# Kernel optimization log

Measured on AMD Instinct MI355X. Metric: run time of the kernel, lower is better.

The kernel has to match this reference:

```python
import jax, jax.numpy as jnp
import numpy as np

BATCH, SEQ, IN, HID, LAYERS = 128, 512, 512, 1024, 2


def setup_inputs() -> dict:
    key = jax.random.key(0)
    ks = jax.random.split(key, 8)
    s = 0.02
    # Gate weights concatenated in order [forget, input, output, cell]
    W0 = jax.random.normal(ks[0], (IN + HID, 4 * HID), dtype=jnp.float32) * s
    b0 = jax.random.normal(ks[1], (4 * HID,), dtype=jnp.float32) * s
    W1 = jax.random.normal(ks[2], (HID + HID, 4 * HID), dtype=jnp.float32) * s
    b1 = jax.random.normal(ks[3], (4 * HID,), dtype=jnp.float32) * s
    Wout = jax.random.normal(ks[4], (HID, 1), dtype=jnp.float32) * s
    bout = jax.random.normal(ks[5], (1,), dtype=jnp.float32) * s
    x = jax.random.normal(ks[6], (BATCH, SEQ, IN), dtype=jnp.float32)
    return {"x": x, "W0": W0, "b0": b0, "W1": W1, "b1": b1,
            "Wout": Wout, "bout": bout}


def _cell(x_in, h_prev, c_prev, W, b):
    z = jnp.concatenate([x_in, h_prev], axis=-1) @ W + b  # (B, 4H)
    f, i, o, g = jnp.split(z, 4, axis=-1)
    c_next = jax.nn.sigmoid(f) * c_prev + jax.nn.sigmoid(i) * jnp.tanh(g)
    h_next = jax.nn.sigmoid(o) * jnp.tanh(c_next)
    return h_next, c_next


def reference(x, W0, b0, W1, b1, Wout, bout):
    B = x.shape[0]
    H = W0.shape[1] // 4
    params = ((W0, b0), (W1, b1))

    h0 = tuple(jnp.zeros((B, H), x.dtype) for _ in range(LAYERS))
    c0 = tuple(jnp.zeros((B, H), x.dtype) for _ in range(LAYERS))

    def step(carry, x_t):
        h, c = carry
        inp = x_t
        new_h, new_c = [], []
        for l in range(LAYERS):
            W, b = params[l]
            h_n, c_n = _cell(inp, h[l], c[l], W, b)
            new_h.append(h_n)
            new_c.append(c_n)
            inp = h_n
        return (tuple(new_h), tuple(new_c)), None

    xs = jnp.swapaxes(x, 0, 1)  # (T, B, IN)
    (h_fin, _), _ = jax.lax.scan(step, (h0, c0), xs)
    last = h_fin[-1]  # output of top layer at last timestep
    logits = last @ Wout + bout  # (B, 1)
    return jax.nn.sigmoid(logits).squeeze(-1)  # (B,)
```

## Files before the change

### kernel.cpp

```cpp
#include <hip/hip_runtime.h>
#include <hip/hip_bf16.h>
#include <cstdint>
#include <cstddef>


#define BATCH 128
#define SEQ   512
#define INP   512
#define HID   1024
#define NCOL  4096
#define NB    256
#define KS0   48
#define KS1   64
#define HS_   (BATCH * HID)

typedef __bf16 bf16x8 __attribute__((ext_vector_type(8)));
typedef float  f32x4  __attribute__((ext_vector_type(4)));
typedef unsigned int u32x4 __attribute__((ext_vector_type(4)));
typedef unsigned long long u64;
typedef u64 u64x2 __attribute__((ext_vector_type(2)));

__device__ __forceinline__ bf16x8 load_bf16x8(const __hip_bfloat16* p) {
    u32x4 u = *reinterpret_cast<const u32x4*>(p);
    return __builtin_bit_cast(bf16x8, u);
}
__device__ __forceinline__ bf16x8 aload_bf16x8(const __hip_bfloat16* p) {
    u64x2 q;
    q[0] = __hip_atomic_load((const u64*)p,       __ATOMIC_RELAXED, __HIP_MEMORY_SCOPE_AGENT);
    q[1] = __hip_atomic_load((const u64*)(p + 4), __ATOMIC_RELAXED, __HIP_MEMORY_SCOPE_AGENT);
    return __builtin_bit_cast(bf16x8, q);
}
__device__ __forceinline__ f32x4 mfma16(bf16x8 a, bf16x8 b, f32x4 c) {
    return __builtin_amdgcn_mfma_f32_16x16x32_bf16(a, b, c, 0, 0, 0);
}
__device__ __forceinline__ float sigmoidf_(float x) {
    return 1.0f / (1.0f + __expf(-x));
}
__device__ __forceinline__ float tanhf_(float x) {
    return 1.0f - 2.0f / (__expf(2.0f * x) + 1.0f);
}
__device__ __forceinline__ void gload16(const void* g, void* l) {
    __builtin_amdgcn_global_load_lds(
        (const __attribute__((address_space(1))) uint32_t*)g,
        (__attribute__((address_space(3))) uint32_t*)l, 16, 0, 0);
}
#define VMWAIT asm volatile("s_waitcnt vmcnt(12)" ::: "memory")

template<int Ks>
__global__ __launch_bounds__(1024)
void pack_frag_kernel(const float* __restrict__ W, __hip_bfloat16* __restrict__ F)
{
    __shared__ float tile[32][33];
    const int k0 = blockIdx.x * 32;
    const int c0 = blockIdx.y * 32;
    const int tx = threadIdx.x & 31, ty = threadIdx.x >> 5;
    tile[ty][tx] = W[(size_t)(k0 + ty) * NCOL + (c0 + tx)];
    __syncthreads();
    const int cL  = threadIdx.x >> 5;
    const int kgw = (threadIdx.x >> 3) & 3;
    const int j   = threadIdx.x & 7;
    const int c   = c0 + cL;
    const int r   = (c & 1023) * 4 + (c >> 10);
    const int nb2 = r >> 4, cl = r & 15;
    const int ks  = k0 >> 5;
    const size_t chunk = ((size_t)(nb2 * Ks + ks) * 4 + kgw) * 16 + cl;
    F[chunk * 8 + j] = __float2bfloat16(tile[kgw * 8 + j][cL]);
}

__global__ void bias_reorder_kernel(const float* __restrict__ b0,
                                    const float* __restrict__ b1,
                                    float* __restrict__ b0r,
                                    float* __restrict__ b1r)
{
    int i = blockIdx.x * blockDim.x + threadIdx.x;
    if (i >= 2 * NCOL) return;
    const float* src = (i < NCOL) ? b0 : b1;
    float*       dst = (i < NCOL) ? b0r : b1r;
    int c = i & (NCOL - 1);
    dst[(c & 1023) * 4 + (c >> 10)] = src[c];
}

__global__ __launch_bounds__(256)
void xconv_kernel(const float* __restrict__ x, __hip_bfloat16* __restrict__ xb)
{
    const int idx = blockIdx.x * 256 + threadIdx.x;
    const int r   = idx & 63;
    const int kg  = (idx >> 6) & 3;
    const int mq  = (idx >> 8) & 1;
    const int ks  = (idx >> 9) & 15;
    const int t   = idx >> 13;
    const float* src = x + ((size_t)(mq * 64 + r) * SEQ + t) * INP + ks * 32 + kg * 8;
    bf16x8 v;
    #pragma unroll
    for (int j = 0; j < 8; ++j) v[j] = (__bf16)src[j];
    *reinterpret_cast<u32x4*>(xb + (size_t)idx * 8) = __builtin_bit_cast(u32x4, v);
}

__global__ __launch_bounds__(512, 2)
void lstm_persistent(const __hip_bfloat16* __restrict__ xb,
                     const __hip_bfloat16* __restrict__ F0,
                     const __hip_bfloat16* __restrict__ F1,
                     const float* __restrict__ b0r,
                     const float* __restrict__ b1r,
                     const float* __restrict__ Wout,
                     const float* __restrict__ bout,
                     __hip_bfloat16* __restrict__ h0r,
                     __hip_bfloat16* __restrict__ h1r,
                     float* __restrict__ out,
                     int* __restrict__ bar,
                     int rm, int fm)
{
    extern __shared__ char smem[];

    __shared__ float zacc[2][128][17];
    __shared__ float cS[2][512];
    __shared__ float biasS[2][16];
    __shared__ __hip_bfloat16 hstage[2][128][4];

    const int tid  = threadIdx.x;
    const int lane = tid & 63;
    const int wv   = tid >> 6;
    const int kq   = wv & 3;
    const int mq   = wv >> 2;
    const int lm   = lane & 15;
    const int kg   = lane >> 4;
    const int nb   = blockIdx.x;
    const uint32_t sbase = (uint32_t)wv * 16384;

    bf16x8 B0r_[12], B1r_[16];
    #pragma unroll
    for (int i = 0; i < 4; ++i)
        B0r_[i]     = load_bf16x8(F0 + ((((size_t)nb * KS0 + (4*kq + i)) * 4 + kg) * 16 + lm) * 8);
    #pragma unroll
    for (int i = 0; i < 8; ++i)
        B0r_[4 + i] = load_bf16x8(F0 + ((((size_t)nb * KS0 + (16 + 8*kq + i)) * 4 + kg) * 16 + lm) * 8);
    #pragma unroll
    for (int i = 0; i < 8; ++i)
        B1r_[i]     = load_bf16x8(F1 + ((((size_t)nb * KS1 + (8*kq + i)) * 4 + kg) * 16 + lm) * 8);
    #pragma unroll
    for (int i = 0; i < 8; ++i)
        B1r_[8 + i] = load_bf16x8(F1 + ((((size_t)nb * KS1 + (32 + 8*kq + i)) * 4 + kg) * 16 + lm) * 8);

    #pragma unroll
    for (int i = 0; i < 12; ++i) asm volatile("" : "+v"(B0r_[i]));
    #pragma unroll
    for (int i = 0; i < 16; ++i) asm volatile("" : "+v"(B1r_[i]));

    if (tid < 32) biasS[tid >> 4][tid & 15] = ((tid < 16) ? b0r : b1r)[nb * 16 + (tid & 15)];
    for (int i = tid; i < 1024; i += 512) cS[i >> 9][i & 511] = 0.f;
    for (int i = tid; i < 2 * 128 * 17; i += 512) ((float*)zacc)[i] = 0.f;
    __syncthreads();

    auto issueStep = [&](const __hip_bfloat16* src, int sl) {
        const char* g = (const char*)src + (size_t)lane * 16;
        char* l = smem + sbase + (uint32_t)sl * 4096;
        #pragma unroll
        for (int i2 = 0; i2 < 4; ++i2)
            gload16(g + i2 * 1024, l + i2 * 1024);
    };
    auto readA = [&](int sl, int f) -> bf16x8 {
        const char* lp = smem + sbase + (uint32_t)sl * 4096
                       + (uint32_t)kg * 1024 + (uint32_t)f * 256 + (uint32_t)lm * 16;
        u32x4 v = *(const u32x4*)lp;
        return __builtin_bit_cast(bf16x8, v);
    };

    #pragma unroll
    for (int s = 0; s < 4; ++s)
        issueStep(xb + ((size_t)((4*kq + s) * 2 + mq)) * 2048, s);

    for (int p = 0; p <= SEQ; ++p) {
        const __hip_bfloat16* h0p = h0r + (size_t)((p + rm)     & rm) * HS_;
        const __hip_bfloat16* h1p = h1r + (size_t)((p + rm - 1) & rm) * HS_;
        __hip_bfloat16*       h0w = h0r + (size_t)( p           & rm) * HS_;
        __hip_bfloat16*       h1w = h1r + (size_t)((p + rm)     & rm) * HS_;
        const int tn = (p + 1 < SEQ) ? (p + 1) : (SEQ - 1);

        f32x4 aL0[4], aL1[4];
        #pragma unroll
        for (int f = 0; f < 4; ++f) { aL0[f] = f32x4{0,0,0,0}; aL1[f] = f32x4{0,0,0,0}; }

        #pragma unroll
        for (int s = 0; s < 4; ++s) {
            VMWAIT;
            bf16x8 A[4];
            #pragma unroll
            for (int f = 0; f < 4; ++f) A[f] = readA(s, f);
            #pragma unroll
            for (int f = 0; f < 4; ++f) aL0[f] = mfma16(A[f], B0r_[s], aL0[f]);
            issueStep(h0p + ((size_t)((8*kq + s) * 2 + mq)) * 2048, s);
        }
        #pragma unroll
        for (int i = 0; i < 8; ++i) {
            VMWAIT;
            const int sl = (4 + i) & 3;
            bf16x8 A[4];
            #pragma unroll
            for (int f = 0; f < 4; ++f) A[f] = readA(sl, f);
            #pragma unroll
            for (int f = 0; f < 4; ++f) {
                aL0[f] = mfma16(A[f], B0r_[4 + i], aL0[f]);
                aL1[f] = mfma16(A[f], B1r_[i],     aL1[f]);
            }
            if (i < 4) issueStep(h0p + ((size_t)((8*kq + 4 + i)   * 2 + mq)) * 2048, (8 + i) & 3);
            else       issueStep(h1p + ((size_t)((8*kq + (i - 4)) * 2 + mq)) * 2048, (8 + i) & 3);
        }
        #pragma unroll
        for (int i = 0; i < 8; ++i) {
            VMWAIT;
            const int sl = (12 + i) & 3;
            bf16x8 A[4];
            #pragma unroll
            for (int f = 0; f < 4; ++f) A[f] = readA(sl, f);
            #pragma unroll
            for (int f = 0; f < 4; ++f) aL1[f] = mfma16(A[f], B1r_[8 + i], aL1[f]);
            if (i < 4)
                issueStep(h1p + ((size_t)((8*kq + 4 + i) * 2 + mq)) * 2048, (16 + i) & 3);
            else if (p < SEQ)
                issueStep(xb + (size_t)tn * 65536
                             + ((size_t)((4*kq + (i - 4)) * 2 + mq)) * 2048, (16 + i) & 3);
        }

        if (p < SEQ) {
            #pragma unroll
            for (int f = 0; f < 4; ++f)
                #pragma unroll
                for (int r = 0; r < 4; ++r)
                    atomicAdd(&zacc[0][mq*64 + f*16 + kg*4 + r][lm], aL0[f][r]);
        }
        if (p >= 1) {
            #pragma unroll
            for (int f = 0; f < 4; ++f)
                #pragma unroll
                for (int r = 0; r < 4; ++r)
                    atomicAdd(&zacc[1][mq*64 + f*16 + kg*4 + r][lm], aL1[f][r]);
        }
        __syncthreads();

        for (int it = tid; it < 1024; it += 512) {
            const int L   = it >> 9;
            const int idx = it & 511;
            const int bl  = idx >> 2;
            const int u   = idx & 3;
            const bool act = L ? (p >= 1) : (p < SEQ);
            if (act) {
                float* zb = &zacc[L][bl][4 * u];
                const float zf = zb[0] + biasS[L][4*u + 0];
                const float zi = zb[1] + biasS[L][4*u + 1];
                const float zo = zb[2] + biasS[L][4*u + 2];
                const float zg = zb[3] + biasS[L][4*u + 3];
                zb[0] = 0.f; zb[1] = 0.f; zb[2] = 0.f; zb[3] = 0.f;
                const float cold = cS[L][idx];
                const float cn = sigmoidf_(zf) * cold + sigmoidf_(zi) * tanhf_(zg);
                const float hn = sigmoidf_(zo) * tanhf_(cn);
                cS[L][idx] = cn;
                hstage[L][bl][u] = __float2bfloat16(hn);
            }
        }
        __syncthreads();

        if (tid < 256) {
            const int L  = tid >> 7;
            const int bl = tid & 127;
            const bool act = L ? (p >= 1) : (p < SEQ);
            if (act) {
                __hip_bfloat16* hw = L ? h1w : h0w;
                const int uks = nb >> 3, ukg = (nb >> 1) & 3, jb = (nb & 1) * 4;
                const int mqb = bl >> 6, rr = bl & 63;
                const size_t e = ((size_t)((uks*2 + mqb)*4 + ukg)*64 + rr)*8 + jb;
                const u64 v = *(const u64*)&hstage[L][bl][0];
                __hip_atomic_store((u64*)(hw + e), v,
                                   __ATOMIC_RELAXED, __HIP_MEMORY_SCOPE_AGENT);
            }
        }
        __syncthreads();

        if (tid == 0) {
            const int g = nb >> 5;
            int* arrv = bar + 32 * g;
            int* root = bar + 256;
            int* rel  = bar + 512 + 32 * g;
            const int e = p + 1;
            __hip_atomic_fetch_add(arrv, 1, __ATOMIC_RELAXED, __HIP_MEMORY_SCOPE_AGENT);
            if ((nb & 31) == 0) {
                while (__hip_atomic_load(arrv, __ATOMIC_RELAXED, __HIP_MEMORY_SCOPE_AGENT) < 32 * e)
                    __builtin_amdgcn_s_sleep(1);
                __hip_atomic_fetch_add(root, 1, __ATOMIC_RELAXED, __HIP_MEMORY_SCOPE_AGENT);
            }
            if (nb == 0) {
                while (__hip_atomic_load(root, __ATOMIC_RELAXED, __HIP_MEMORY_SCOPE_AGENT) < 8 * e)
                    __builtin_amdgcn_s_sleep(1);
                #pragma unroll
                for (int gg = 0; gg < 8; ++gg)
                    __hip_atomic_store(bar + 512 + 32 * gg, e,
                                       __ATOMIC_RELAXED, __HIP_MEMORY_SCOPE_AGENT);
            } else {
                while (__hip_atomic_load(rel, __ATOMIC_RELAXED, __HIP_MEMORY_SCOPE_AGENT) < e)
                    __builtin_amdgcn_s_sleep(2);
            }
            if ((p & fm) == fm)
                __builtin_amdgcn_fence(__ATOMIC_ACQUIRE, "agent");
            asm volatile("" ::: "memory");
        }
        __builtin_amdgcn_s_barrier();
    }

    if (nb == 0 && tid < BATCH) {
        const __hip_bfloat16* hb = h1r + (size_t)((SEQ - 1) & rm) * HS_;
        const int mqb = tid >> 6, rr = tid & 63;
        float acc = 0.f;
        for (int uu = 0; uu < HID; uu += 8) {
            const int uks = uu >> 5, ukg = (uu >> 3) & 3;
            const size_t e = ((size_t)((uks*2 + mqb)*4 + ukg)*64 + rr)*8;
            bf16x8 v = aload_bf16x8(hb + e);
            #pragma unroll
            for (int j = 0; j < 8; ++j) acc += (float)v[j] * Wout[uu + j];
        }
        out[tid] = 1.f / (1.f + __expf(-(acc + bout[0])));
    }
}

extern "C" void kernel_launch(void* const* d_in, const int* in_sizes, int n_in,
                              void* d_out, int out_size, void* d_ws, size_t ws_size,
                              hipStream_t stream)
{
    const float* x    = (const float*)d_in[0];
    const float* W0   = (const float*)d_in[1];
    const float* b0   = (const float*)d_in[2];
    const float* W1   = (const float*)d_in[3];
    const float* b1   = (const float*)d_in[4];
    const float* Wout = (const float*)d_in[5];
    const float* bout = (const float*)d_in[6];
    float* out = (float*)d_out;

    char* ws = (char*)d_ws;
    const size_t OFF_F0  = 0;
    const size_t OFF_F1  = 12582912;
    const size_t OFF_B0R = 29360128;
    const size_t OFF_B1R = 29376512;
    const size_t OFF_BAR = 29392896;
    const size_t OFF_R0  = 29396992;
    const size_t SLOT    = 262144;
    const size_t XBYTES  = (size_t)BATCH * SEQ * INP * 2;

    int rm, fm;
    if      (ws_size >= OFF_R0 + 128 * SLOT + XBYTES) { rm = 63; fm = 31; }
    else if (ws_size >= OFF_R0 +  32 * SLOT + XBYTES) { rm = 15; fm = 7;  }
    else                                              { rm = 1;  fm = 0;  }
    const size_t OFF_R1 = OFF_R0 + (size_t)(rm + 1) * SLOT;
    const size_t OFF_XB = OFF_R1 + (size_t)(rm + 1) * SLOT;

    __hip_bfloat16* F0  = (__hip_bfloat16*)(ws + OFF_F0);
    __hip_bfloat16* F1  = (__hip_bfloat16*)(ws + OFF_F1);
    float* b0r = (float*)(ws + OFF_B0R);
    float* b1r = (float*)(ws + OFF_B1R);
    __hip_bfloat16* h0r = (__hip_bfloat16*)(ws + OFF_R0);
    __hip_bfloat16* h1r = (__hip_bfloat16*)(ws + OFF_R1);
    int* bar = (int*)(ws + OFF_BAR);
    __hip_bfloat16* xbp = (__hip_bfloat16*)(ws + OFF_XB);

    hipMemsetAsync(ws + OFF_BAR, 0, 4096, stream);
    hipMemsetAsync(ws + OFF_R0 + (size_t)rm * SLOT, 0, SLOT, stream);
    hipMemsetAsync(ws + OFF_R1 + (size_t)rm * SLOT, 0, SLOT, stream);

    pack_frag_kernel<KS0><<<dim3(48, 128), 1024, 0, stream>>>(W0, F0);
    pack_frag_kernel<KS1><<<dim3(64, 128), 1024, 0, stream>>>(W1, F1);
    bias_reorder_kernel<<<32, 256, 0, stream>>>(b0, b1, b0r, b1r);
    xconv_kernel<<<(BATCH * SEQ * INP) / (256 * 8), 256, 0, stream>>>(x, xbp);

    hipFuncSetAttribute((const void*)lstm_persistent,
                        hipFuncAttributeMaxDynamicSharedMemorySize, 131072);

    void* args[] = {(void*)&xbp, (void*)&F0, (void*)&F1, (void*)&b0r, (void*)&b1r,
                    (void*)&Wout, (void*)&bout, (void*)&h0r, (void*)&h1r,
                    (void*)&out, (void*)&bar, (void*)&rm, (void*)&fm};
    hipLaunchCooperativeKernel((void*)lstm_persistent, dim3(NB), dim3(512),
                               args, 131072, stream);
}
```

Measured before the change: 15.32 ms.

## Split grid barrier into arrive/wait to overlap x-projection MFMAs with sync

The per-step grid barrier becomes split-phase. Each block signals arrival right after writing its hidden state, then computes the input-projection MFMAs for the next step (which need only x, already prefetched) before waiting on the release. This hides part of the barrier latency behind independent work. The final output block now waits for all arrivals explicitly, and the next-x prefetch is no longer guarded at the last step. The changed counter thresholds raise some risk of ordering bugs.

```diff
diff --git a/kernel.cpp b/kernel.cpp
--- a/kernel.cpp
+++ b/kernel.cpp
@@ -140,7 +140,6 @@
     #pragma unroll
     for (int i = 0; i < 8; ++i)
         B1r_[8 + i] = load_bf16x8(F1 + ((((size_t)nb * KS1 + (32 + 8*kq + i)) * 4 + kg) * 16 + lm) * 8);
-
     #pragma unroll
     for (int i = 0; i < 12; ++i) asm volatile("" : "+v"(B0r_[i]));
     #pragma unroll
@@ -168,6 +167,7 @@
     #pragma unroll
     for (int s = 0; s < 4; ++s)
         issueStep(xb + ((size_t)((4*kq + s) * 2 + mq)) * 2048, s);
+    asm volatile("s_waitcnt vmcnt(0)" ::: "memory");
 
     for (int p = 0; p <= SEQ; ++p) {
         const __hip_bfloat16* h0p = h0r + (size_t)((p + rm)     & rm) * HS_;
@@ -182,14 +182,43 @@
 
         #pragma unroll
         for (int s = 0; s < 4; ++s) {
-            VMWAIT;
             bf16x8 A[4];
             #pragma unroll
             for (int f = 0; f < 4; ++f) A[f] = readA(s, f);
             #pragma unroll
             for (int f = 0; f < 4; ++f) aL0[f] = mfma16(A[f], B0r_[s], aL0[f]);
+        }
+
+        if (tid == 0) {
+            const int g = nb >> 5;
+            int* arrv = bar + 32 * g;
+            int* root = bar + 256;
+            int* rel  = bar + 512 + 32 * g;
+            if ((nb & 31) == 0) {
+                while (__hip_atomic_load(arrv, __ATOMIC_RELAXED, __HIP_MEMORY_SCOPE_AGENT) < 32 * p)
+                    __builtin_amdgcn_s_sleep(1);
+                __hip_atomic_fetch_add(root, 1, __ATOMIC_RELAXED, __HIP_MEMORY_SCOPE_AGENT);
+            }
+            if (nb == 0) {
+                while (__hip_atomic_load(root, __ATOMIC_RELAXED, __HIP_MEMORY_SCOPE_AGENT) < 8 * (p + 1))
+                    __builtin_amdgcn_s_sleep(1);
+                #pragma unroll
+                for (int gg = 0; gg < 8; ++gg)
+                    __hip_atomic_store(bar + 512 + 32 * gg, p,
+                                       __ATOMIC_RELAXED, __HIP_MEMORY_SCOPE_AGENT);
+            } else {
+                while (__hip_atomic_load(rel, __ATOMIC_RELAXED, __HIP_MEMORY_SCOPE_AGENT) < p)
+                    __builtin_amdgcn_s_sleep(2);
+            }
+            if ((p & fm) == fm)
+                __builtin_amdgcn_fence(__ATOMIC_ACQUIRE, "agent");
+            asm volatile("" ::: "memory");
+        }
+        __builtin_amdgcn_s_barrier();
+
+        #pragma unroll
+        for (int s = 0; s < 4; ++s)
             issueStep(h0p + ((size_t)((8*kq + s) * 2 + mq)) * 2048, s);
-        }
         #pragma unroll
         for (int i = 0; i < 8; ++i) {
             VMWAIT;
@@ -216,7 +245,7 @@
             for (int f = 0; f < 4; ++f) aL1[f] = mfma16(A[f], B1r_[8 + i], aL1[f]);
             if (i < 4)
                 issueStep(h1p + ((size_t)((8*kq + 4 + i) * 2 + mq)) * 2048, (16 + i) & 3);
-            else if (p < SEQ)
+            else
                 issueStep(xb + (size_t)tn * 65536
                              + ((size_t)((4*kq + (i - 4)) * 2 + mq)) * 2048, (16 + i) & 3);
         }
@@ -275,48 +304,33 @@
         }
         __syncthreads();
 
+        if (tid == 0)
+            __hip_atomic_fetch_add(bar + 32 * (nb >> 5), 1,
+                                   __ATOMIC_RELAXED, __HIP_MEMORY_SCOPE_AGENT);
+    }
+
+    if (nb == 0) {
         if (tid == 0) {
-            const int g = nb >> 5;
-            int* arrv = bar + 32 * g;
-            int* root = bar + 256;
-            int* rel  = bar + 512 + 32 * g;
-            const int e = p + 1;
-            __hip_atomic_fetch_add(arrv, 1, __ATOMIC_RELAXED, __HIP_MEMORY_SCOPE_AGENT);
-            if ((nb & 31) == 0) {
-                while (__hip_atomic_load(arrv, __ATOMIC_RELAXED, __HIP_MEMORY_SCOPE_AGENT) < 32 * e)
-                    __builtin_amdgcn_s_sleep(1);
-                __hip_atomic_fetch_add(root, 1, __ATOMIC_RELAXED, __HIP_MEMORY_SCOPE_AGENT);
-            }
-            if (nb == 0) {
-                while (__hip_atomic_load(root, __ATOMIC_RELAXED, __HIP_MEMORY_SCOPE_AGENT) < 8 * e)
-                    __builtin_amdgcn_s_sleep(1);
+            #pragma unroll
+            for (int gg = 0; gg < 8; ++gg)
+                while (__hip_atomic_load(bar + 32 * gg, __ATOMIC_RELAXED,
+                                         __HIP_MEMORY_SCOPE_AGENT) < 32 * (SEQ + 1))
+                    __builtin_amdgcn_s_sleep(2);
+        }
+        __syncthreads();
+        if (tid < BATCH) {
+            const __hip_bfloat16* hb = h1r + (size_t)((SEQ - 1) & rm) * HS_;
+            const int mqb = tid >> 6, rr = tid & 63;
+            float acc = 0.f;
+            for (int uu = 0; uu < HID; uu += 8) {
+                const int uks = uu >> 5, ukg = (uu >> 3) & 3;
+                const size_t e = ((size_t)((uks*2 + mqb)*4 + ukg)*64 + rr)*8;
+                bf16x8 v = aload_bf16x8(hb + e);
                 #pragma unroll
-                for (int gg = 0; gg < 8; ++gg)
-                    __hip_atomic_store(bar + 512 + 32 * gg, e,
-                                       __ATOMIC_RELAXED, __HIP_MEMORY_SCOPE_AGENT);
-            } else {
-                while (__hip_atomic_load(rel, __ATOMIC_RELAXED, __HIP_MEMORY_SCOPE_AGENT) < e)
-                    __builtin_amdgcn_s_sleep(2);
-            }
-            if ((p & fm) == fm)
-                __builtin_amdgcn_fence(__ATOMIC_ACQUIRE, "agent");
-            asm volatile("" ::: "memory");
-        }
-        __builtin_amdgcn_s_barrier();
-    }
-
-    if (nb == 0 && tid < BATCH) {
-        const __hip_bfloat16* hb = h1r + (size_t)((SEQ - 1) & rm) * HS_;
-        const int mqb = tid >> 6, rr = tid & 63;
-        float acc = 0.f;
-        for (int uu = 0; uu < HID; uu += 8) {
-            const int uks = uu >> 5, ukg = (uu >> 3) & 3;
-            const size_t e = ((size_t)((uks*2 + mqb)*4 + ukg)*64 + rr)*8;
-            bf16x8 v = aload_bf16x8(hb + e);
-            #pragma unroll
-            for (int j = 0; j < 8; ++j) acc += (float)v[j] * Wout[uu + j];
-        }
-        out[tid] = 1.f / (1.f + __expf(-(acc + bout[0])));
+                for (int j = 0; j < 8; ++j) acc += (float)v[j] * Wout[uu + j];
+            }
+            out[tid] = 1.f / (1.f + __expf(-(acc + bout[0])));
+        }
     }
 }
 
```

Measured after the change: 15.23 ms. About the same (-0.6%).
